# Optimization experiments

Measured on AMD Instinct MI355X. Metric: run time of the kernel, lower is better.

The kernel has to match this reference:

```python
import jax, jax.numpy as jnp
import numpy as np

EPS = 1e-5


def conv1x1(x, w):
    # x: (N, C, V, T), w: (O, C) -> (N, O, V, T)
    return jnp.einsum('ncvt,oc->novt', x, w)


def batchnorm2d(y, gamma, beta):
    # training-mode BN over (N, V, T) per channel, biased variance (torch semantics)
    mean = jnp.mean(y, axis=(0, 2, 3), keepdims=True)
    var = jnp.mean((y - mean) ** 2, axis=(0, 2, 3), keepdims=True)
    yhat = (y - mean) * jax.lax.rsqrt(var + EPS)
    return yhat * gamma[None, :, None, None] + beta[None, :, None, None]


def spatial_g(x, wg1, wg2):
    # learned adjacency: softmax over last dim of (N, T, V, V)
    a1 = conv1x1(x, wg1)  # (N, O, V, T)
    a2 = conv1x1(x, wg2)  # (N, O, V, T)
    g = jnp.einsum('novt,nout->ntvu', a1, a2)  # (N, T, V, V)
    return jax.nn.softmax(g, axis=-1)


def gcn_unit(x, g, w1, w2, gamma, beta):
    # message passing: g (N,T,V,V) applied over joint dim of x (N,C,V,T)
    x1 = jnp.einsum('ntvu,ncut->ncvt', g, x)
    y = conv1x1(x1, w1) + conv1x1(x, w2)
    return jax.nn.relu(batchnorm2d(y, gamma, beta))


def setup_inputs() -> dict:
    key = jax.random.key(0)
    ks = jax.random.split(key, 12)
    N, C, V, T = 64, 64, 25, 128
    dims = [64, 64, 128, 256]
    gp = 16
    s = 0.05
    inp = {
        'x': jax.random.normal(ks[0], (N, C, V, T), jnp.float32),
        'wg1': jax.random.normal(ks[1], (gp, dims[0]), jnp.float32) * s,
        'wg2': jax.random.normal(ks[2], (gp, dims[0]), jnp.float32) * s,
        'w11': jax.random.normal(ks[3], (dims[1], dims[0]), jnp.float32) * s,
        'w12': jax.random.normal(ks[4], (dims[1], dims[0]), jnp.float32) * s,
        'gamma1': jnp.ones((dims[1],), jnp.float32),
        'beta1': jnp.zeros((dims[1],), jnp.float32),
        'w21': jax.random.normal(ks[5], (dims[2], dims[1]), jnp.float32) * s,
        'w22': jax.random.normal(ks[6], (dims[2], dims[1]), jnp.float32) * s,
        'gamma2': jnp.ones((dims[2],), jnp.float32),
        'beta2': jnp.zeros((dims[2],), jnp.float32),
        'w31': jax.random.normal(ks[7], (dims[3], dims[2]), jnp.float32) * s,
        'w32': jax.random.normal(ks[8], (dims[3], dims[2]), jnp.float32) * s,
        'gamma3': jnp.ones((dims[3],), jnp.float32),
        'beta3': jnp.zeros((dims[3],), jnp.float32),
    }
    return inp


def reference(x, wg1, wg2, w11, w12, gamma1, beta1, w21, w22, gamma2, beta2,
              w31, w32, gamma3, beta3):
    g = spatial_g(x, wg1, wg2)                       # shared adjacency (N,T,V,V)
    x = gcn_unit(x, g, w11, w12, gamma1, beta1)      # (N, 64, V, T)
    x = gcn_unit(x, g, w21, w22, gamma2, beta2)      # (N, 128, V, T)
    x = gcn_unit(x, g, w31, w32, gamma3, beta3)      # (N, 256, V, T)
    return x, g
```

## Files before the change

### kernel.cpp

```cpp
#include <hip/hip_runtime.h>
#include <cstdint>

#define V_ 25
#define T_ 128
#define VT_ 3200
#define NVTF_ 204800.0f

typedef unsigned short ushort_t;
typedef __attribute__((ext_vector_type(8))) short s16x8;
typedef __attribute__((ext_vector_type(4))) short s16x4;
typedef __attribute__((ext_vector_type(4))) float f32x4;

__device__ __forceinline__ ushort_t f2bf(float f) {
    union { float f; unsigned u; } v; v.f = f;
    unsigned r = v.u + 0x7FFFu + ((v.u >> 16) & 1u);
    return (ushort_t)(r >> 16);
}
__device__ __forceinline__ float bf2f(ushort_t h) {
    union { unsigned u; float f; } v; v.u = ((unsigned)h) << 16;
    return v.f;
}
__device__ __forceinline__ unsigned cvtpk(float lo, float hi) {
    unsigned r;
    asm volatile("v_cvt_pk_bf16_f32 %0, %1, %2" : "=v"(r) : "v"(lo), "v"(hi));
    return r;
}
__device__ __forceinline__ void gload16(const void* g, void* l) {
    __builtin_amdgcn_global_load_lds((const __attribute__((address_space(1))) void*)g,
                                     (__attribute__((address_space(3))) void*)l, 16, 0, 0);
}

__global__ __launch_bounds__(128) void k_a(const float* __restrict__ x,
        const float* __restrict__ wg1, const float* __restrict__ wg2,
        ushort_t* __restrict__ a1, ushort_t* __restrict__ a2,
        ushort_t* __restrict__ xb,
        const float* __restrict__ w11, const float* __restrict__ w12,
        const float* __restrict__ w21, const float* __restrict__ w22,
        const float* __restrict__ w31, const float* __restrict__ w32,
        ushort_t* __restrict__ Wc) {
    int b = blockIdx.x; int n = b / V_; int v = b % V_;
    int t = threadIdx.x;
    int wi = b * 128 + t;
    if (wi < 90112) {
        float wv;
        if (wi < 8192) {
            int o = wi >> 7, k = wi & 127;
            wv = (k < 64) ? w11[o * 64 + k] : w12[o * 64 + k - 64];
        } else if (wi < 24576) {
            int j = wi - 8192; int o = j >> 7, k = j & 127;
            wv = (k < 64) ? w21[o * 64 + k] : w22[o * 64 + k - 64];
        } else {
            int j = wi - 24576; int o = j >> 8, k = j & 255;
            wv = (k < 128) ? w31[o * 128 + k] : w32[o * 128 + k - 128];
        }
        Wc[wi] = f2bf(wv);
    }
    __shared__ float w1s[1024], w2s[1024];
    for (int i = threadIdx.x; i < 1024; i += 128) { w1s[i] = wg1[i]; w2s[i] = wg2[i]; }
    __syncthreads();
    float s1[16], s2[16];
    #pragma unroll
    for (int o = 0; o < 16; o++) { s1[o] = 0.f; s2[o] = 0.f; }
    s16x8 xs[8];
    const float* xp = x + (size_t)n * 204800 + v * T_ + t;
    #pragma unroll
    for (int c = 0; c < 64; c++) {
        float xv = xp[(size_t)c * VT_];
        xs[c >> 3][c & 7] = (short)f2bf(xv);
        #pragma unroll
        for (int o = 0; o < 16; o++) {
            s1[o] = fmaf(w1s[o*64+c], xv, s1[o]);
            s2[o] = fmaf(w2s[o*64+c], xv, s2[o]);
        }
    }
    size_t abase = (size_t)n * 51200 + v * T_ + t;
    #pragma unroll
    for (int o = 0; o < 16; o++) {
        a1[abase + (size_t)o * VT_] = f2bf(s1[o]);
        a2[abase + (size_t)o * VT_] = f2bf(s2[o]);
    }
    ushort_t* cp = xb + (size_t)(n * VT_ + v * T_ + t) * 64;
    #pragma unroll
    for (int ch = 0; ch < 8; ch++) *(s16x8*)(cp + ch * 8) = xs[ch];
}

__global__ __launch_bounds__(256) void k_g(const ushort_t* __restrict__ a1,
        const ushort_t* __restrict__ a2, float* __restrict__ g,
        ushort_t* __restrict__ gb) {
    int n = blockIdx.x >> 3; int t0 = (blockIdx.x & 7) * 16;
    __shared__ float A1s[6400], A2s[6400];
    for (int i = threadIdx.x; i < 6400; i += 256) {
        int o = i / 400; int r = i % 400; int v = r >> 4; int tt = r & 15;
        size_t ga = (size_t)n * 51200 + (size_t)o * VT_ + v * T_ + t0 + tt;
        A1s[i] = bf2f(a1[ga]);
        A2s[i] = bf2f(a2[ga]);
    }
    __syncthreads();
    for (int r = threadIdx.x; r < 400; r += 256) {
        int v = r >> 4; int tt = r & 15;
        float a1r[16];
        #pragma unroll
        for (int o = 0; o < 16; o++) a1r[o] = A1s[o*400 + v*16 + tt];
        float gr[25];
        float mx = -1e30f;
        for (int u = 0; u < 25; u++) {
            float s = 0.f;
            #pragma unroll
            for (int o = 0; o < 16; o++) s = fmaf(a1r[o], A2s[o*400 + u*16 + tt], s);
            gr[u] = s; mx = fmaxf(mx, s);
        }
        float sum = 0.f;
        for (int u = 0; u < 25; u++) { gr[u] = __expf(gr[u] - mx); sum += gr[u]; }
        float inv = 1.f / sum;
        float* gp = g + ((size_t)(n * T_ + t0 + tt) * V_ + v) * V_;
        ushort_t* gbp = gb + ((size_t)((n * 128 + t0 + tt) * 25 + v)) * 32;
        for (int u = 0; u < 25; u++) {
            float val = gr[u] * inv;
            gp[u] = val;
            gbp[u] = f2bf(val);
        }
    }
}

template<int C, bool BNB, bool XBSRC, int TOUT, int OPASS>
__global__ __launch_bounds__(256) void k_fgemm(
        const ushort_t* __restrict__ Wc, const ushort_t* __restrict__ ysrc,
        const ushort_t* __restrict__ gb,
        const float* __restrict__ bns, const float* __restrict__ bnb,
        ushort_t* __restrict__ yt,
        float* __restrict__ psum, float* __restrict__ psq) {
    constexpr int K2 = 2 * C;
    constexpr int KSTEPS = K2 / 32;
    constexpr int NC8 = C / 8;
    constexpr int HKS = C / 32;
    constexpr int MROWS = 100;
    constexpr int MI = 7;
    constexpr int CW = (C == 64) ? 1 : 2;
    constexpr int XBYTES = (TOUT == 0) ? 14400 : 13824;
    __shared__ __align__(16) ushort_t YS[MROWS * C];
    __shared__ __align__(16) ushort_t MPo[MROWS * C];
    __shared__ __align__(16) char XTRA[XBYTES];
    float* GS = (float*)XTRA;
    ushort_t* Lw = (ushort_t*)XTRA;

    int n = blockIdx.y, mb = blockIdx.x;
    int m0 = mb * MROWS, tb = mb * 4;
    int tid = threadIdx.x, w = tid >> 6, lane = tid & 63;
    int l15 = lane & 15, g4 = lane >> 4;

    for (int i = tid; i < 2500; i += 256) {
        int tl = i / 625, r = i % 625, u = r / 25, v = r % 25;
        GS[(tl * 25 + u) * 28 + v] =
            bf2f(gb[((size_t)((n * 128 + tb + tl) * 25 + v)) * 32 + u]);
    }
    for (int i = tid; i < MROWS * NC8; i += 256) {
        int yr = i / NC8, cc = i % NC8;
        size_t saddr;
        if (XBSRC) {
            int t = tb + yr / 25, v = yr % 25;
            saddr = (size_t)n * 204800 + (size_t)(v * 128 + t) * 64 + cc * 8;
        } else {
            saddr = ((size_t)n * VT_ + m0 + yr) * C + cc * 8;
        }
        s16x8 vv = *(const s16x8*)(ysrc + saddr);
        if (BNB) {
            int ob = cc * 8;
            float4 s0 = *(const float4*)(bns + ob), s1 = *(const float4*)(bns + ob + 4);
            float4 h0 = *(const float4*)(bnb + ob), h1 = *(const float4*)(bnb + ob + 4);
            float sc[8] = {s0.x, s0.y, s0.z, s0.w, s1.x, s1.y, s1.z, s1.w};
            float sh[8] = {h0.x, h0.y, h0.z, h0.w, h1.x, h1.y, h1.z, h1.w};
            float ff[8];
            #pragma unroll
            for (int j = 0; j < 8; j++)
                ff[j] = fmaxf(fmaf(bf2f((ushort_t)vv[j]), sc[j], sh[j]), 0.f);
            union { unsigned u[4]; s16x8 s; } U;
            U.u[0] = cvtpk(ff[0], ff[1]); U.u[1] = cvtpk(ff[2], ff[3]);
            U.u[2] = cvtpk(ff[4], ff[5]); U.u[3] = cvtpk(ff[6], ff[7]);
            vv = U.s;
        }
        *(s16x8*)(YS + ((size_t)yr * NC8 + (cc ^ (yr & 7))) * 8) = vv;
    }
    __syncthreads();
    {
        int cwi = tid & 63;
        int tl = tid >> 6;
        int c8 = (cwi * CW) >> 3;
        int sub = (cwi * CW) & 7;
        float macc[25][CW];
        #pragma unroll
        for (int v = 0; v < 25; v++)
            #pragma unroll
            for (int k = 0; k < CW; k++) macc[v][k] = 0.f;
        for (int u = 0; u < 25; u++) {
            int yr = tl * 25 + u;
            const ushort_t* yp = YS + ((size_t)yr * NC8 + (c8 ^ (yr & 7))) * 8 + sub;
            float yf[CW];
            if (CW == 2) {
                unsigned yw = *(const unsigned*)yp;
                yf[0] = bf2f((ushort_t)(yw & 0xFFFFu));
                yf[1] = bf2f((ushort_t)(yw >> 16));
            } else {
                yf[0] = bf2f(*yp);
            }
            const float* gp = &GS[(tl * 25 + u) * 28];
            float gv[25];
            #pragma unroll
            for (int q = 0; q < 6; q++) {
                float4 gq = *(const float4*)(gp + q * 4);
                gv[q*4+0] = gq.x; gv[q*4+1] = gq.y; gv[q*4+2] = gq.z; gv[q*4+3] = gq.w;
            }
            gv[24] = gp[24];
            #pragma unroll
            for (int v = 0; v < 25; v++)
                #pragma unroll
                for (int k = 0; k < CW; k++)
                    macc[v][k] = fmaf(gv[v], yf[k], macc[v][k]);
        }
        #pragma unroll
        for (int v = 0; v < 25; v++) {
            int r = tl * 25 + v;
            ushort_t* op = MPo + ((size_t)r * NC8 + (c8 ^ (r & 7))) * 8 + sub;
            if (CW == 2) {
                *(unsigned*)op = cvtpk(macc[v][0], macc[v][1]);
            } else {
                *op = f2bf(macc[v][0]);
            }
        }
    }
    __syncthreads();
    for (int pass = 0; pass < OPASS; pass++) {
        int o0 = pass * 64;
        s16x8 aReg[KSTEPS];
        const ushort_t* ap = Wc + (size_t)(o0 + w * 16 + l15) * K2 + g4 * 8;
        #pragma unroll
        for (int ks = 0; ks < KSTEPS; ks++)
            aReg[ks] = *(const s16x8*)(ap + ks * 32);
        f32x4 acc[MI] = {};
        __builtin_amdgcn_s_setprio(1);
        #pragma unroll
        for (int ks = 0; ks < KSTEPS; ks++) {
            const ushort_t* bbase = (ks < HKS) ? MPo : YS;
            int ksl = (ks < HKS) ? ks : ks - HKS;
            #pragma unroll
            for (int mi = 0; mi < MI; mi++) {
                int r = mi * 16 + l15;
                int rr = (r < MROWS) ? r : (MROWS - 1);
                int ch = ksl * 4 + g4;
                s16x8 bF = *(const s16x8*)(bbase + ((size_t)rr * NC8 + (ch ^ (rr & 7))) * 8);
                acc[mi] = __builtin_amdgcn_mfma_f32_16x16x32_bf16(aReg[ks], bF, acc[mi], 0, 0, 0);
            }
        }
        __builtin_amdgcn_s_setprio(0);
        int p = n * 32 + mb;
        #pragma unroll
        for (int b = 0; b < 4; b++) {
            float ss = 0.f, qq = 0.f;
            #pragma unroll
            for (int mi = 0; mi < MI; mi++) {
                float v0 = acc[mi][b];
                if (mi == 6 && l15 >= 4) v0 = 0.f;
                ss += v0; qq = fmaf(v0, v0, qq);
            }
            #pragma unroll
            for (int msk = 1; msk < 16; msk <<= 1) {
                ss += __shfl_xor(ss, msk, 16);
                qq += __shfl_xor(qq, msk, 16);
            }
            if (l15 == 0) {
                int o = o0 + w * 16 + g4 * 4 + b;
                psum[(size_t)o * 2048 + p] = ss;
                psq [(size_t)o * 2048 + p] = qq;
            }
        }
        if (TOUT == 0) {
            __syncthreads();
            #pragma unroll
            for (int mi = 0; mi < MI; mi++) {
                int r = mi * 16 + l15;
                if (r < MROWS) {
                    unsigned lo = cvtpk(acc[mi][0], acc[mi][1]);
                    unsigned hi = cvtpk(acc[mi][2], acc[mi][3]);
                    *(unsigned*)(Lw + r * 72 + w * 16 + g4 * 4)     = lo;
                    *(unsigned*)(Lw + r * 72 + w * 16 + g4 * 4 + 2) = hi;
                }
            }
            __syncthreads();
            for (int i = tid; i < MROWS * 8; i += 256) {
                int r = i >> 3, oc = i & 7;
                s16x8 pk = *(const s16x8*)(Lw + r * 72 + oc * 8);
                *(s16x8*)(yt + ((size_t)n * VT_ + m0 + r) * (OPASS * 64) + o0 + oc * 8) = pk;
            }
        } else {
            __syncthreads();
            #pragma unroll
            for (int mi = 0; mi < MI; mi++) {
                int r = mi * 16 + l15;
                if (r < MROWS) {
                    int ol = w * 16 + g4 * 4;
                    Lw[(ol + 0) * 108 + r] = f2bf(acc[mi][0]);
                    Lw[(ol + 1) * 108 + r] = f2bf(acc[mi][1]);
                    Lw[(ol + 2) * 108 + r] = f2bf(acc[mi][2]);
                    Lw[(ol + 3) * 108 + r] = f2bf(acc[mi][3]);
                }
            }
            __syncthreads();
            for (int i = tid; i < 64 * 25; i += 256) {
                int ol = i / 25, mc = i % 25;
                s16x4 pk = *(const s16x4*)(Lw + ol * 108 + mc * 4);
                *(s16x4*)(yt + (size_t)(n * 256 + o0 + ol) * VT_ + m0 + mc * 4) = pk;
            }
        }
    }
}

__global__ __launch_bounds__(256) void k_stats(const float* __restrict__ psum,
        const float* __restrict__ psq, const float* __restrict__ gamma,
        const float* __restrict__ beta, float* __restrict__ bns,
        float* __restrict__ bnb) {
    int o = blockIdx.x;
    float s = 0.f, q = 0.f;
    for (int i = threadIdx.x; i < 2048; i += 256) {
        s += psum[(size_t)o*2048+i]; q += psq[(size_t)o*2048+i];
    }
    __shared__ float rs[256], rq[256];
    rs[threadIdx.x] = s; rq[threadIdx.x] = q;
    __syncthreads();
    for (int st = 128; st > 0; st >>= 1) {
        if (threadIdx.x < st) { rs[threadIdx.x] += rs[threadIdx.x+st]; rq[threadIdx.x] += rq[threadIdx.x+st]; }
        __syncthreads();
    }
    if (threadIdx.x == 0) {
        float mean = rs[0] / NVTF_;
        float var = rq[0] / NVTF_ - mean * mean;
        float scale = gamma[o] * rsqrtf(var + 1e-5f);
        bns[o] = scale;
        bnb[o] = beta[o] - mean * scale;
    }
}

__global__ __launch_bounds__(256) void k_bnf(const ushort_t* __restrict__ y3,
        const float* __restrict__ bns, const float* __restrict__ bnb,
        float* __restrict__ xout) {
    __shared__ __align__(16) ushort_t L[8 * VT_];
    int n = blockIdx.y, oc = blockIdx.x;
    size_t base = (size_t)(n * 256 + oc * 8) * VT_;
    for (int i = threadIdx.x; i < 3200; i += 256)
        gload16(y3 + base + (size_t)i * 8, (char*)L + i * 16);
    __syncthreads();
    for (int i = threadIdx.x; i < 6400; i += 256) {
        int t4 = i & 31, v = (i >> 5) % 25, o = i / 800;
        int og = oc * 8 + o;
        float sc = bns[og], sh = bnb[og];
        int lb = o * VT_ + v;
        float4 f;
        f.x = fmaxf(fmaf(bf2f(L[lb + (t4*4+0)*25]), sc, sh), 0.f);
        f.y = fmaxf(fmaf(bf2f(L[lb + (t4*4+1)*25]), sc, sh), 0.f);
        f.z = fmaxf(fmaf(bf2f(L[lb + (t4*4+2)*25]), sc, sh), 0.f);
        f.w = fmaxf(fmaf(bf2f(L[lb + (t4*4+3)*25]), sc, sh), 0.f);
        *(float4*)(xout + (size_t)(n * 256 + og) * VT_ + v * T_ + t4 * 4) = f;
    }
}

extern "C" void kernel_launch(void* const* d_in, const int* in_sizes, int n_in,
                              void* d_out, int out_size, void* d_ws, size_t ws_size,
                              hipStream_t stream) {
    const float* x   = (const float*)d_in[0];
    const float* wg1 = (const float*)d_in[1];
    const float* wg2 = (const float*)d_in[2];
    const float* w11 = (const float*)d_in[3];
    const float* w12 = (const float*)d_in[4];
    const float* ga1 = (const float*)d_in[5];
    const float* be1 = (const float*)d_in[6];
    const float* w21 = (const float*)d_in[7];
    const float* w22 = (const float*)d_in[8];
    const float* ga2 = (const float*)d_in[9];
    const float* be2 = (const float*)d_in[10];
    const float* w31 = (const float*)d_in[11];
    const float* w32 = (const float*)d_in[12];
    const float* ga3 = (const float*)d_in[13];
    const float* be3 = (const float*)d_in[14];

    float* xout = (float*)d_out;
    float* gout = xout + 52428800;

    float* ws = (float*)d_ws;
    ushort_t* xb  = (ushort_t*)(ws + 0);
    ushort_t* a1  = (ushort_t*)(ws + 6553600);
    ushort_t* a2  = (ushort_t*)(ws + 8192000);
    ushort_t* y1  = (ushort_t*)(ws + 9830400);
    ushort_t* y2  = (ushort_t*)(ws + 16384000);
    ushort_t* y3  = (ushort_t*)(ws + 29491200);
    ushort_t* gb  = (ushort_t*)(ws + 55705600);
    float* psum = ws + 58982400;
    float* psq  = ws + 59506688;
    ushort_t* Wc = (ushort_t*)(ws + 60030976);
    float* bns  = ws + 60076032;
    float* bnb  = ws + 60076288;
    ushort_t* Wc1 = Wc, *Wc2 = Wc + 8192, *Wc3 = Wc + 24576;

    k_a<<<1600, 128, 0, stream>>>(x, wg1, wg2, a1, a2, xb,
                                  w11, w12, w21, w22, w31, w32, Wc);
    k_g<<<512, 256, 0, stream>>>(a1, a2, gout, gb);

    k_fgemm<64, false, true, 0, 1><<<dim3(32, 64), 256, 0, stream>>>(
        Wc1, xb, gb, nullptr, nullptr, y1, psum, psq);
    k_stats<<<64, 256, 0, stream>>>(psum, psq, ga1, be1, bns, bnb);

    k_fgemm<64, true, false, 0, 2><<<dim3(32, 64), 256, 0, stream>>>(
        Wc2, y1, gb, bns, bnb, y2, psum, psq);
    k_stats<<<128, 256, 0, stream>>>(psum, psq, ga2, be2, bns, bnb);

    k_fgemm<128, true, false, 2, 4><<<dim3(32, 64), 256, 0, stream>>>(
        Wc3, y2, gb, bns, bnb, y3, psum, psq);
    k_stats<<<256, 256, 0, stream>>>(psum, psq, ga3, be3, bns, bnb);

    k_bnf<<<dim3(32, 64), 256, 0, stream>>>(y3, bns, bnb, xout);
}
```

Before: 347.8 us.

## Compute graph message passing with MFMA and write TOUT output directly

Replaces the scalar FMA graph aggregation (g applied over joints) with bf16 16x16x32 MFMA instructions that read the adjacency straight from global memory, padding the bf16 adjacency rows with zeros for u 25..31. The LDS swizzle is extended to also XOR with row bits 3..5, to reduce bank conflicts for the new strided per-element B-fragment gathers. The transposed output path drops its LDS staging and writes scalar bf16 values directly to global memory. This cuts LDS use and VALU work, but the transposed stores become uncoalesced 2-byte writes and the gathers read LDS one element at a time.

Result: faster. 292.1 us (-16.0%).

```diff
diff --git a/kernel.cpp b/kernel.cpp
--- a/kernel.cpp
+++ b/kernel.cpp
@@ -8,8 +8,9 @@
 
 typedef unsigned short ushort_t;
 typedef __attribute__((ext_vector_type(8))) short s16x8;
-typedef __attribute__((ext_vector_type(4))) short s16x4;
 typedef __attribute__((ext_vector_type(4))) float f32x4;
+
+#define SW(r, ch) ((ch) ^ ((r) & 7) ^ (((r) >> 3) & 7))
 
 __device__ __forceinline__ ushort_t f2bf(float f) {
     union { float f; unsigned u; } v; v.f = f;
@@ -119,6 +120,8 @@
             gp[u] = val;
             gbp[u] = f2bf(val);
         }
+        #pragma unroll
+        for (int u = 25; u < 32; u++) gbp[u] = 0;
     }
 }
 
@@ -132,15 +135,14 @@
     constexpr int K2 = 2 * C;
     constexpr int KSTEPS = K2 / 32;
     constexpr int NC8 = C / 8;
+    constexpr int NCT = C / 16;
     constexpr int HKS = C / 32;
     constexpr int MROWS = 100;
     constexpr int MI = 7;
-    constexpr int CW = (C == 64) ? 1 : 2;
-    constexpr int XBYTES = (TOUT == 0) ? 14400 : 13824;
+    constexpr int XBYTES = (TOUT == 0) ? 14400 : 16;
     __shared__ __align__(16) ushort_t YS[MROWS * C];
     __shared__ __align__(16) ushort_t MPo[MROWS * C];
     __shared__ __align__(16) char XTRA[XBYTES];
-    float* GS = (float*)XTRA;
     ushort_t* Lw = (ushort_t*)XTRA;
 
     int n = blockIdx.y, mb = blockIdx.x;
@@ -148,11 +150,6 @@
     int tid = threadIdx.x, w = tid >> 6, lane = tid & 63;
     int l15 = lane & 15, g4 = lane >> 4;
 
-    for (int i = tid; i < 2500; i += 256) {
-        int tl = i / 625, r = i % 625, u = r / 25, v = r % 25;
-        GS[(tl * 25 + u) * 28 + v] =
-            bf2f(gb[((size_t)((n * 128 + tb + tl) * 25 + v)) * 32 + u]);
-    }
     for (int i = tid; i < MROWS * NC8; i += 256) {
         int yr = i / NC8, cc = i % NC8;
         size_t saddr;
@@ -178,52 +175,39 @@
             U.u[2] = cvtpk(ff[4], ff[5]); U.u[3] = cvtpk(ff[6], ff[7]);
             vv = U.s;
         }
-        *(s16x8*)(YS + ((size_t)yr * NC8 + (cc ^ (yr & 7))) * 8) = vv;
+        *(s16x8*)(YS + ((size_t)yr * NC8 + SW(yr, cc)) * 8) = vv;
     }
     __syncthreads();
     {
-        int cwi = tid & 63;
-        int tl = tid >> 6;
-        int c8 = (cwi * CW) >> 3;
-        int sub = (cwi * CW) & 7;
-        float macc[25][CW];
-        #pragma unroll
-        for (int v = 0; v < 25; v++)
-            #pragma unroll
-            for (int k = 0; k < CW; k++) macc[v][k] = 0.f;
-        for (int u = 0; u < 25; u++) {
-            int yr = tl * 25 + u;
-            const ushort_t* yp = YS + ((size_t)yr * NC8 + (c8 ^ (yr & 7))) * 8 + sub;
-            float yf[CW];
-            if (CW == 2) {
-                unsigned yw = *(const unsigned*)yp;
-                yf[0] = bf2f((ushort_t)(yw & 0xFFFFu));
-                yf[1] = bf2f((ushort_t)(yw >> 16));
-            } else {
-                yf[0] = bf2f(*yp);
-            }
-            const float* gp = &GS[(tl * 25 + u) * 28];
-            float gv[25];
-            #pragma unroll
-            for (int q = 0; q < 6; q++) {
-                float4 gq = *(const float4*)(gp + q * 4);
-                gv[q*4+0] = gq.x; gv[q*4+1] = gq.y; gv[q*4+2] = gq.z; gv[q*4+3] = gq.w;
-            }
-            gv[24] = gp[24];
-            #pragma unroll
-            for (int v = 0; v < 25; v++)
-                #pragma unroll
-                for (int k = 0; k < CW; k++)
-                    macc[v][k] = fmaf(gv[v], yf[k], macc[v][k]);
-        }
-        #pragma unroll
-        for (int v = 0; v < 25; v++) {
-            int r = tl * 25 + v;
-            ushort_t* op = MPo + ((size_t)r * NC8 + (c8 ^ (r & 7))) * 8 + sub;
-            if (CW == 2) {
-                *(unsigned*)op = cvtpk(macc[v][0], macc[v][1]);
-            } else {
-                *op = f2bf(macc[v][0]);
+        int tl = w;
+        const ushort_t* gbase = gb + ((size_t)((n * 128 + tb + tl) * 25)) * 32;
+        s16x8 aG0 = *(const s16x8*)(gbase + (size_t)(l15) * 32 + g4 * 8);
+        s16x8 aG1 = *(const s16x8*)(gbase + (size_t)(16 + l15) * 32 + g4 * 8);
+        #pragma unroll
+        for (int ct = 0; ct < NCT; ct++) {
+            int c = ct * 16 + l15;
+            int cc = c >> 3, sub = c & 7;
+            s16x8 bF;
+            #pragma unroll
+            for (int j = 0; j < 8; j++) {
+                int u = g4 * 8 + j;
+                int uu = (u > 24) ? 24 : u;
+                int r = tl * 25 + uu;
+                bF[j] = (short)YS[((size_t)r * NC8 + SW(r, cc)) * 8 + sub];
+            }
+            f32x4 z = {};
+            f32x4 d0 = __builtin_amdgcn_mfma_f32_16x16x32_bf16(aG0, bF, z, 0, 0, 0);
+            f32x4 d1 = __builtin_amdgcn_mfma_f32_16x16x32_bf16(aG1, bF, z, 0, 0, 0);
+            #pragma unroll
+            for (int b = 0; b < 4; b++) {
+                int v0 = g4 * 4 + b;
+                int r0 = tl * 25 + v0;
+                MPo[((size_t)r0 * NC8 + SW(r0, cc)) * 8 + sub] = f2bf(d0[b]);
+                int v1 = 16 + g4 * 4 + b;
+                if (v1 < 25) {
+                    int r1 = tl * 25 + v1;
+                    MPo[((size_t)r1 * NC8 + SW(r1, cc)) * 8 + sub] = f2bf(d1[b]);
+                }
             }
         }
     }
@@ -246,7 +230,7 @@
                 int r = mi * 16 + l15;
                 int rr = (r < MROWS) ? r : (MROWS - 1);
                 int ch = ksl * 4 + g4;
-                s16x8 bF = *(const s16x8*)(bbase + ((size_t)rr * NC8 + (ch ^ (rr & 7))) * 8);
+                s16x8 bF = *(const s16x8*)(bbase + ((size_t)rr * NC8 + SW(rr, ch)) * 8);
                 acc[mi] = __builtin_amdgcn_mfma_f32_16x16x32_bf16(aReg[ks], bF, acc[mi], 0, 0, 0);
             }
         }
@@ -291,23 +275,15 @@
                 *(s16x8*)(yt + ((size_t)n * VT_ + m0 + r) * (OPASS * 64) + o0 + oc * 8) = pk;
             }
         } else {
-            __syncthreads();
+            int obase = n * 256 + o0 + w * 16 + g4 * 4;
             #pragma unroll
             for (int mi = 0; mi < MI; mi++) {
                 int r = mi * 16 + l15;
                 if (r < MROWS) {
-                    int ol = w * 16 + g4 * 4;
-                    Lw[(ol + 0) * 108 + r] = f2bf(acc[mi][0]);
-                    Lw[(ol + 1) * 108 + r] = f2bf(acc[mi][1]);
-                    Lw[(ol + 2) * 108 + r] = f2bf(acc[mi][2]);
-                    Lw[(ol + 3) * 108 + r] = f2bf(acc[mi][3]);
+                    #pragma unroll
+                    for (int b = 0; b < 4; b++)
+                        yt[(size_t)(obase + b) * VT_ + m0 + r] = f2bf(acc[mi][b]);
                 }
-            }
-            __syncthreads();
-            for (int i = tid; i < 64 * 25; i += 256) {
-                int ol = i / 25, mc = i % 25;
-                s16x4 pk = *(const s16x4*)(Lw + ol * 108 + mc * 4);
-                *(s16x4*)(yt + (size_t)(n * 256 + o0 + ol) * VT_ + m0 + mc * 4) = pk;
             }
         }
     }
```
